# Optimization experiments

Hardware: AMD Instinct MI355X
Metric: run time of the kernel (lower is better)

The kernel has to match this reference:

```python
import jax, jax.numpy as jnp
import numpy as np

B, N, D = 32, 1024, 512
NUM_CLASSES = 4
LN_EPS = 1e-5


def _layer_norm(x, g, b):
    mu = jnp.mean(x, axis=-1, keepdims=True)
    var = jnp.mean(jnp.square(x - mu), axis=-1, keepdims=True)
    return (x - mu) * jax.lax.rsqrt(var + LN_EPS) * g + b


def setup_inputs() -> dict:
    key = jax.random.key(0)
    ks = jax.random.split(key, 8)
    s = 0.05
    inp = {
        "sc_matrix": jax.random.uniform(ks[0], (B, N, N), dtype=jnp.float32),
        # GCN encoder params
        "W1": jax.random.normal(ks[1], (N, D), dtype=jnp.float32) * s,
        "b1": jnp.zeros((D,), jnp.float32),
        "W2": jax.random.normal(ks[2], (D, D), dtype=jnp.float32) * s,
        "b2": jnp.zeros((D,), jnp.float32),
        "ln_g": jnp.ones((D,), jnp.float32),
        "ln_b": jnp.zeros((D,), jnp.float32),
        # classifier params
        "Wc1": jax.random.normal(ks[3], (D, 128), dtype=jnp.float32) * s,
        "bc1": jnp.zeros((128,), jnp.float32),
        "g1": jnp.ones((128,), jnp.float32),
        "t1": jnp.zeros((128,), jnp.float32),
        "Wc2": jax.random.normal(ks[4], (128, 64), dtype=jnp.float32) * s,
        "bc2": jnp.zeros((64,), jnp.float32),
        "g2": jnp.ones((64,), jnp.float32),
        "t2": jnp.zeros((64,), jnp.float32),
        "Wc3": jax.random.normal(ks[5], (64, NUM_CLASSES), dtype=jnp.float32) * s,
        "bc3": jnp.zeros((NUM_CLASSES,), jnp.float32),
    }
    return inp


def reference(sc_matrix, W1, b1, W2, b2, ln_g, ln_b,
              Wc1, bc1, g1, t1, Wc2, bc2, g2, t2, Wc3, bc3):
    # Every entry of sc_matrix is nonzero, so the edge list covers all (i,j)
    # pairs incl. self-loops; GCN message passing == dense normalized matmul.
    # PyG gcn_norm: deg[j] = sum_i A[i,j]; out = D^-1/2 A^T D^-1/2 h.
    A = sc_matrix                              # [B,N,N], A[b,i,j] = edge i->j
    deg = jnp.sum(A, axis=-2)                  # col sums, [B,N]
    dis = jnp.where(deg > 0, jax.lax.rsqrt(deg), 0.0)   # deg^{-1/2}
    An = jnp.swapaxes(A, -1, -2) * dis[:, :, None] * dis[:, None, :]  # [B,N,N]

    x = sc_matrix                              # node features = SC rows [B,N,N]
    h = jax.nn.relu(jnp.matmul(An, jnp.matmul(x, W1)) + b1)   # conv1+relu [B,N,D]
    h = jnp.matmul(An, jnp.matmul(h, W2)) + b2                # conv2      [B,N,D]
    z = _layer_norm(h, ln_g, ln_b)

    z_pooled = jnp.mean(z, axis=1)             # [B,D]

    c = jax.nn.relu(_layer_norm(z_pooled @ Wc1 + bc1, g1, t1))
    c = jax.nn.relu(_layer_norm(c @ Wc2 + bc2, g2, t2))
    logits = c @ Wc3 + bc3                     # [B,num_classes]
    return (logits, z_pooled)
```

## Files before the change

### kernel.cpp

```cpp
#include <hip/hip_runtime.h>
#include <hip/hip_bf16.h>

#define B_ 32
#define N_ 1024
#define D_ 512
#define LN_EPS 1e-5f

using bf16 = __bf16;
using bf16x4 = __attribute__((ext_vector_type(4))) __bf16;
using bf16x8 = __attribute__((ext_vector_type(8))) __bf16;
using floatx4 = __attribute__((ext_vector_type(4))) float;

__device__ __forceinline__ void gld16(const bf16* gp, bf16* lp) {
  __builtin_amdgcn_global_load_lds(
      (const __attribute__((address_space(1))) void*)gp,
      (__attribute__((address_space(3))) void*)lp, 16, 0, 0);
}

__global__ __launch_bounds__(256) void k_pre(const float* __restrict__ A,
                                             float* __restrict__ deg_part,
                                             bf16* __restrict__ Abf,
                                             const float* __restrict__ W1,
                                             bf16* __restrict__ W1t,
                                             const float* __restrict__ W2,
                                             bf16* __restrict__ W2t) {
  int blk = blockIdx.x;
  int t = threadIdx.x;
  if (blk < 512) {
    int b = blk >> 4;
    int rc = blk & 15;
    int r0 = rc * 64;
    const float* p = A + (size_t)b * N_ * N_ + (size_t)r0 * N_ + t * 4;
    bf16* op = Abf + (size_t)b * N_ * N_ + (size_t)r0 * N_ + t * 4;
    float4 acc = {0.f, 0.f, 0.f, 0.f};
    #pragma unroll 4
    for (int i = 0; i < 64; ++i) {
      float4 v = *(const float4*)(p + (size_t)i * N_);
      acc.x += v.x; acc.y += v.y; acc.z += v.z; acc.w += v.w;
      bf16x4 o = {(bf16)v.x, (bf16)v.y, (bf16)v.z, (bf16)v.w};
      *(bf16x4*)(op + (size_t)i * N_) = o;
    }
    *(float4*)(deg_part + ((size_t)rc * B_ + b) * N_ + t * 4) = acc;
  } else {
    __shared__ float tile[64][65];
    blk -= 512;
    const float* in; bf16* outp; int R, C, c0, r0;
    if (blk < 128) {
      in = W1; outp = W1t; R = N_; C = D_;
      c0 = (blk & 7) * 64; r0 = (blk >> 3) * 64;
    } else {
      blk -= 128;
      in = W2; outp = W2t; R = D_; C = D_;
      c0 = (blk & 7) * 64; r0 = (blk >> 3) * 64;
    }
    #pragma unroll
    for (int cc = 0; cc < 4; ++cc) {
      int idx = cc * 256 + t;
      int r = idx >> 4, c4 = (idx & 15) << 2;
      const float4 v = *(const float4*)(in + (size_t)(r0 + r) * C + c0 + c4);
      tile[r][c4 + 0] = v.x; tile[r][c4 + 1] = v.y;
      tile[r][c4 + 2] = v.z; tile[r][c4 + 3] = v.w;
    }
    __syncthreads();
    #pragma unroll
    for (int cc = 0; cc < 4; ++cc) {
      int idx = cc * 256 + t;
      int c = idx >> 4, r4 = (idx & 15) << 2;
      bf16* dst = outp + (size_t)(c0 + c) * R + r0 + r4;
      #pragma unroll
      for (int e = 0; e < 4; ++e) dst[e] = (bf16)tile[r4 + e][c];
    }
  }
}

__global__ __launch_bounds__(256) void k_build(const bf16* __restrict__ Abf,
                                               const float* __restrict__ deg_part,
                                               bf16* __restrict__ Anbf) {
  __shared__ float tile[64][65];
  __shared__ float disI[64], disJ[64];
  int b = blockIdx.z;
  int i0 = blockIdx.x * 64;
  int j0 = blockIdx.y * 64;
  int t = threadIdx.x;
  const bf16* Ab = Abf + (size_t)b * N_ * N_;
  bf16* Anb = Anbf + (size_t)b * N_ * N_;
  if (t < 64) {
    float v = 0.f;
    #pragma unroll
    for (int rc = 0; rc < 16; ++rc)
      v += deg_part[((size_t)rc * B_ + b) * N_ + i0 + t];
    disI[t] = v > 0.f ? rsqrtf(v) : 0.f;
  } else if (t < 128) {
    float v = 0.f;
    #pragma unroll
    for (int rc = 0; rc < 16; ++rc)
      v += deg_part[((size_t)rc * B_ + b) * N_ + j0 + (t - 64)];
    disJ[t - 64] = v > 0.f ? rsqrtf(v) : 0.f;
  }
  #pragma unroll
  for (int cc = 0; cc < 2; ++cc) {
    int idx = cc * 256 + t;
    int r = idx >> 3;
    int c8 = (idx & 7) << 3;
    bf16x8 v = *(const bf16x8*)(Ab + (size_t)(j0 + r) * N_ + i0 + c8);
    #pragma unroll
    for (int e = 0; e < 8; ++e) tile[r][c8 + e] = (float)v[e];
  }
  __syncthreads();
  #pragma unroll
  for (int cc = 0; cc < 2; ++cc) {
    int idx = cc * 256 + t;
    int ii = idx >> 3;
    int jj8 = (idx & 7) << 3;
    float di = disI[ii];
    bf16x8 o;
    #pragma unroll
    for (int e = 0; e < 8; ++e)
      o[e] = (bf16)(tile[jj8 + e][ii] * di * disJ[jj8 + e]);
    *(bf16x8*)(Anb + (size_t)(i0 + ii) * N_ + j0 + jj8) = o;
  }
}

template <bool BIAS, bool RELU>
__global__ __launch_bounds__(512, 2) void k_gemm8(
    const bf16* __restrict__ Abase, size_t strideA,
    const bf16* __restrict__ Btbase, size_t strideBt,
    bf16* __restrict__ Cbase, size_t strideC,
    const float* __restrict__ bias, int Nn, int K) {
  __shared__ __align__(16) bf16 smem[65536];
  bf16* sAp = smem;
  bf16* sBp = smem + 32768;

  int nxy = gridDim.x * gridDim.y;
  int L = blockIdx.z * nxy + blockIdx.y * gridDim.x + blockIdx.x;
  int b = (L & 7) + 8 * (L / (nxy * 8));
  int inner = (L >> 3) % nxy;
  int n0 = (inner % gridDim.x) * 256;
  int m0 = (inner / gridDim.x) * 256;
  const bf16* A = Abase + (size_t)b * strideA;
  const bf16* Bt = Btbase + (size_t)b * strideBt;
  int t = threadIdx.x;
  int lane = t & 63;
  int wid = t >> 6;
  int wm = wid >> 2, wn = wid & 3;
  int l16 = lane & 15, q = lane >> 4;
  int xorb = l16 & 7;
  int ck0 = ((q ^ xorb) << 3);
  int ck1 = (((q + 4) ^ xorb) << 3);
  int r0 = t >> 3;
  int csrc = (((t & 7) ^ (r0 & 7)) << 3);
  const bf16* ag = A + (size_t)(m0 + r0) * K + csrc;
  const bf16* bg = Bt + (size_t)(n0 + ((r0 >> 5) << 6) + (r0 & 31)) * K + csrc;
  bf16* al = sAp + (size_t)t * 8;
  bf16* bl = sBp + (size_t)t * 8;

#define STAGE_A(bf_, hf_, kt_)                                                 \
  { gld16(ag + (size_t)((hf_) * 64) * K + (kt_),                               \
          al + (bf_) * 16384 + (hf_) * 8192);                                  \
    gld16(ag + (size_t)(128 + (hf_) * 64) * K + (kt_),                         \
          al + (bf_) * 16384 + (hf_) * 8192 + 4096); }
#define STAGE_B(bf_, hf_, kt_)                                                 \
  { gld16(bg + (size_t)((hf_) * 32) * K + (kt_),                               \
          bl + (bf_) * 16384 + (hf_) * 8192);                                  \
    gld16(bg + (size_t)(128 + (hf_) * 32) * K + (kt_),                         \
          bl + (bf_) * 16384 + (hf_) * 8192 + 4096); }

  floatx4 acc[8][4];
  #pragma unroll
  for (int i = 0; i < 8; ++i)
    #pragma unroll
    for (int j = 0; j < 4; ++j) acc[i][j] = (floatx4){0.f, 0.f, 0.f, 0.f};

  bf16x8 a[4][2];
  bf16x8 bq[4][2];
  const bf16* arow = sAp + (wm * 64 + l16) * 64;
  const bf16* brow = sBp + (wn * 32 + l16) * 64;

#define RD_A(bf_, mq_)                                                         \
  _Pragma("unroll") for (int i = 0; i < 4; ++i) {                              \
    a[i][0] = *(const bf16x8*)(arow + (bf_) * 16384 + (mq_) * 8192 +           \
                               i * 1024 + ck0);                                \
    a[i][1] = *(const bf16x8*)(arow + (bf_) * 16384 + (mq_) * 8192 +           \
                               i * 1024 + ck1);                                \
  }
#define RD_B(bf_, nq_)                                                         \
  _Pragma("unroll") for (int j = 0; j < 2; ++j) {                              \
    bq[(nq_) * 2 + j][0] = *(const bf16x8*)(brow + (bf_) * 16384 +             \
                                            (nq_) * 8192 + j * 1024 + ck0);    \
    bq[(nq_) * 2 + j][1] = *(const bf16x8*)(brow + (bf_) * 16384 +             \
                                            (nq_) * 8192 + j * 1024 + ck1);    \
  }
#define MFMA_Q(mq_, nq_)                                                       \
  _Pragma("unroll") for (int i = 0; i < 4; ++i)                                \
    _Pragma("unroll") for (int j = 0; j < 2; ++j) {                            \
      acc[(mq_) * 4 + i][(nq_) * 2 + j] =                                      \
          __builtin_amdgcn_mfma_f32_16x16x32_bf16(                             \
              a[i][0], bq[(nq_) * 2 + j][0],                                   \
              acc[(mq_) * 4 + i][(nq_) * 2 + j], 0, 0, 0);                     \
      acc[(mq_) * 4 + i][(nq_) * 2 + j] =                                      \
          __builtin_amdgcn_mfma_f32_16x16x32_bf16(                             \
              a[i][1], bq[(nq_) * 2 + j][1],                                   \
              acc[(mq_) * 4 + i][(nq_) * 2 + j], 0, 0, 0);                     \
    }
#define BARRIER __builtin_amdgcn_s_barrier()
#define LGKM0                                                                  \
  do {                                                                         \
    asm volatile("s_waitcnt lgkmcnt(0)" ::: "memory");                         \
    __builtin_amdgcn_sched_barrier(0);                                         \
  } while (0)
#define VMCNT(n_) asm volatile("s_waitcnt vmcnt(" #n_ ")" ::: "memory")

  STAGE_A(0, 0, 0); STAGE_B(0, 0, 0); STAGE_A(0, 1, 0); STAGE_B(0, 1, 0);
  STAGE_A(1, 0, 64); STAGE_B(1, 0, 64);
  VMCNT(4);
  BARRIER;
  int NI = K >> 7;
  for (int it = 0; it < NI; ++it) {
    int kb = it << 7;
    int k1 = kb + 64;
    int k2 = kb + 128; bool p2 = k2 < K;
    int k3 = kb + 192; bool p3 = k3 < K;
    bool lastit = (it == NI - 1);
    RD_A(0, 0); RD_B(0, 0);
    STAGE_A(1, 1, k1);
    BARRIER; LGKM0;
    __builtin_amdgcn_s_setprio(1); MFMA_Q(0, 0); __builtin_amdgcn_s_setprio(0);
    BARRIER;
    RD_B(0, 1);
    STAGE_B(1, 1, k1);
    BARRIER; LGKM0;
    __builtin_amdgcn_s_setprio(1); MFMA_Q(0, 1); __builtin_amdgcn_s_setprio(0);
    BARRIER;
    RD_A(0, 1);
    if (p2) STAGE_A(0, 0, k2);
    BARRIER; LGKM0;
    __builtin_amdgcn_s_setprio(1); MFMA_Q(1, 0); __builtin_amdgcn_s_setprio(0);
    BARRIER;
    if (p2) STAGE_B(0, 0, k2);
    if (lastit) { VMCNT(0); } else { VMCNT(4); }
    BARRIER; LGKM0;
    __builtin_amdgcn_s_setprio(1); MFMA_Q(1, 1); __builtin_amdgcn_s_setprio(0);
    BARRIER;
    RD_A(1, 0); RD_B(1, 0);
    if (p2) STAGE_A(0, 1, k2);
    BARRIER; LGKM0;
    __builtin_amdgcn_s_setprio(1); MFMA_Q(0, 0); __builtin_amdgcn_s_setprio(0);
    BARRIER;
    RD_B(1, 1);
    if (p2) STAGE_B(0, 1, k2);
    BARRIER; LGKM0;
    __builtin_amdgcn_s_setprio(1); MFMA_Q(0, 1); __builtin_amdgcn_s_setprio(0);
    BARRIER;
    RD_A(1, 1);
    if (p3) STAGE_A(1, 0, k3);
    BARRIER; LGKM0;
    __builtin_amdgcn_s_setprio(1); MFMA_Q(1, 0); __builtin_amdgcn_s_setprio(0);
    BARRIER;
    if (p3) STAGE_B(1, 0, k3);
    if (lastit) { VMCNT(0); } else { VMCNT(4); }
    BARRIER; LGKM0;
    __builtin_amdgcn_s_setprio(1); MFMA_Q(1, 1); __builtin_amdgcn_s_setprio(0);
    BARRIER;
  }

  bf16* C = Cbase + (size_t)b * strideC;
  #pragma unroll
  for (int h = 0; h < 2; ++h) {
    BARRIER;
    if (wm == h) {
      #pragma unroll
      for (int fm = 0; fm < 8; ++fm)
        #pragma unroll
        for (int fn = 0; fn < 4; ++fn)
          #pragma unroll
          for (int r = 0; r < 4; ++r) {
            float v = acc[fm][fn][r];
            if (BIAS) v += bias[n0 + wn * 64 + fn * 16 + l16];
            if (RELU) v = v > 0.f ? v : 0.f;
            smem[(fm * 16 + q * 4 + r) * 264 + wn * 64 + fn * 16 + l16] =
                (bf16)v;
          }
    }
    BARRIER;
    #pragma unroll
    for (int i = 0; i < 8; ++i) {
      int idx = i * 512 + t;
      int row = idx >> 5;
      int c8 = (idx & 31) << 3;
      bf16x8 vv = *(const bf16x8*)(smem + row * 264 + c8);
      *(bf16x8*)(C + (size_t)(m0 + h * 128 + row) * Nn + n0 + c8) = vv;
    }
  }
#undef STAGE_A
#undef STAGE_B
#undef RD_A
#undef RD_B
#undef MFMA_Q
#undef BARRIER
#undef LGKM0
#undef VMCNT
}

__global__ __launch_bounds__(256) void k_lnpool(const bf16* __restrict__ H2,
                                                const float* __restrict__ g,
                                                const float* __restrict__ be,
                                                float* __restrict__ zp_part) {
  int b = blockIdx.y;
  int rx = blockIdx.x;
  int r0 = rx * 64;
  int t = threadIdx.x, lane = t & 63, w = t >> 6;
  float ge[8], bee[8];
  #pragma unroll
  for (int e = 0; e < 8; ++e) { ge[e] = g[lane * 8 + e]; bee[e] = be[lane * 8 + e]; }
  float acc[8] = {0, 0, 0, 0, 0, 0, 0, 0};
  for (int rr = 0; rr < 16; ++rr) {
    int row = r0 + w * 16 + rr;
    const bf16* p = H2 + ((size_t)b * N_ + row) * D_ + lane * 8;
    bf16x8 hv = *(const bf16x8*)p;
    float x[8];
    float s = 0.f;
    #pragma unroll
    for (int e = 0; e < 8; ++e) { x[e] = (float)hv[e]; s += x[e]; }
    #pragma unroll
    for (int off = 32; off; off >>= 1) s += __shfl_xor(s, off);
    float mu = s * (1.f / 512.f);
    float ss = 0.f;
    #pragma unroll
    for (int e = 0; e < 8; ++e) { float d = x[e] - mu; ss += d * d; }
    #pragma unroll
    for (int off = 32; off; off >>= 1) ss += __shfl_xor(ss, off);
    float rs = rsqrtf(ss * (1.f / 512.f) + LN_EPS);
    #pragma unroll
    for (int e = 0; e < 8; ++e) acc[e] += (x[e] - mu) * rs * ge[e] + bee[e];
  }
  __shared__ float part[4][512];
  #pragma unroll
  for (int e = 0; e < 8; ++e) part[w][lane * 8 + e] = acc[e];
  __syncthreads();
  #pragma unroll
  for (int k = 0; k < 2; ++k) {
    int d = t + k * 256;
    float s4 = part[0][d] + part[1][d] + part[2][d] + part[3][d];
    zp_part[((size_t)rx * B_ + b) * D_ + d] = s4;
  }
}

__global__ __launch_bounds__(128) void k_cls(
    const float* __restrict__ zp_part,
    const float* __restrict__ Wc1, const float* __restrict__ bc1,
    const float* __restrict__ g1, const float* __restrict__ t1,
    const float* __restrict__ Wc2, const float* __restrict__ bc2,
    const float* __restrict__ g2, const float* __restrict__ t2,
    const float* __restrict__ Wc3, const float* __restrict__ bc3,
    float* __restrict__ out) {
  __shared__ float z[512];
  __shared__ float c1s[128];
  __shared__ float c2s[64];
  __shared__ float red[128];
  int b = blockIdx.x, t = threadIdx.x;
  #pragma unroll
  for (int k = 0; k < 4; ++k) {
    int d = t + k * 128;
    float s = 0.f;
    #pragma unroll
    for (int rx = 0; rx < 16; ++rx)
      s += zp_part[((size_t)rx * B_ + b) * D_ + d];
    float v = s * (1.f / 1024.f);
    z[d] = v;
    out[128 + b * 512 + d] = v;
  }
  __syncthreads();
  float y = bc1[t];
  for (int d = 0; d < 512; ++d) y += z[d] * Wc1[d * 128 + t];
  red[t] = y;
  __syncthreads();
  float mu = 0.f;
  for (int k = 0; k < 128; ++k) mu += red[k];
  mu *= (1.f / 128.f);
  float var = 0.f;
  for (int k = 0; k < 128; ++k) { float dd = red[k] - mu; var += dd * dd; }
  var *= (1.f / 128.f);
  float c = (y - mu) * rsqrtf(var + LN_EPS) * g1[t] + t1[t];
  c1s[t] = c > 0.f ? c : 0.f;
  __syncthreads();
  if (t < 64) {
    float y2 = bc2[t];
    for (int k = 0; k < 128; ++k) y2 += c1s[k] * Wc2[k * 64 + t];
    red[t] = y2;
  }
  __syncthreads();
  if (t < 64) {
    float mu2 = 0.f;
    for (int k = 0; k < 64; ++k) mu2 += red[k];
    mu2 *= (1.f / 64.f);
    float v2 = 0.f;
    for (int k = 0; k < 64; ++k) { float dd = red[k] - mu2; v2 += dd * dd; }
    v2 *= (1.f / 64.f);
    float cc = (red[t] - mu2) * rsqrtf(v2 + LN_EPS) * g2[t] + t2[t];
    c2s[t] = cc > 0.f ? cc : 0.f;
  }
  __syncthreads();
  if (t < 4) {
    float y3 = bc3[t];
    for (int k = 0; k < 64; ++k) y3 += c2s[k] * Wc3[k * 4 + t];
    out[b * 4 + t] = y3;
  }
}

extern "C" void kernel_launch(void* const* d_in, const int* in_sizes, int n_in,
                              void* d_out, int out_size, void* d_ws, size_t ws_size,
                              hipStream_t stream) {
  const float* A   = (const float*)d_in[0];
  const float* W1  = (const float*)d_in[1];
  const float* b1  = (const float*)d_in[2];
  const float* W2  = (const float*)d_in[3];
  const float* b2  = (const float*)d_in[4];
  const float* lng = (const float*)d_in[5];
  const float* lnb = (const float*)d_in[6];
  const float* Wc1 = (const float*)d_in[7];
  const float* bc1 = (const float*)d_in[8];
  const float* g1  = (const float*)d_in[9];
  const float* t1  = (const float*)d_in[10];
  const float* Wc2 = (const float*)d_in[11];
  const float* bc2 = (const float*)d_in[12];
  const float* g2  = (const float*)d_in[13];
  const float* t2  = (const float*)d_in[14];
  const float* Wc3 = (const float*)d_in[15];
  const float* bc3 = (const float*)d_in[16];
  float* out = (float*)d_out;

  char* ws = (char*)d_ws;
  size_t off = 0;
  auto alloc = [&](size_t bytes) {
    char* p = ws + off;
    off += (bytes + 255) & ~(size_t)255;
    return p;
  };
  float* deg_part = (float*)alloc((size_t)16 * B_ * N_ * 4);
  float* zp_part  = (float*)alloc((size_t)16 * B_ * D_ * 4);
  bf16* Anbf  = (bf16*)alloc((size_t)B_ * N_ * N_ * 2);
  bf16* W1t   = (bf16*)alloc((size_t)D_ * N_ * 2);
  bf16* W2t   = (bf16*)alloc((size_t)D_ * D_ * 2);
  bf16* T12t  = (bf16*)alloc((size_t)B_ * D_ * N_ * 2);
  bf16* H1    = (bf16*)alloc((size_t)B_ * N_ * D_ * 2);
  bf16* Abf   = (bf16*)alloc((size_t)B_ * N_ * N_ * 2);
  bf16* H2    = Abf;


  k_pre<<<704, 256, 0, stream>>>(A, deg_part, Abf, W1, W1t, W2, W2t);
  k_build<<<dim3(16, 16, B_), 256, 0, stream>>>(Abf, deg_part, Anbf);

  k_gemm8<false, false><<<dim3(4, 2, B_), 512, 0, stream>>>(
      W1t, 0, Abf, (size_t)N_ * N_, T12t, (size_t)D_ * N_, nullptr, N_, N_);
  k_gemm8<true, true><<<dim3(2, 4, B_), 512, 0, stream>>>(
      Anbf, (size_t)N_ * N_, T12t, (size_t)D_ * N_, H1, (size_t)N_ * D_, b1, D_, N_);
  k_gemm8<false, false><<<dim3(4, 2, B_), 512, 0, stream>>>(
      W2t, 0, H1, (size_t)N_ * D_, T12t, (size_t)D_ * N_, nullptr, N_, D_);
  k_gemm8<true, false><<<dim3(2, 4, B_), 512, 0, stream>>>(
      Anbf, (size_t)N_ * N_, T12t, (size_t)D_ * N_, H2, (size_t)N_ * D_, b2, D_, N_);

  k_lnpool<<<dim3(16, B_), 256, 0, stream>>>(H2, lng, lnb, zp_part);
  k_cls<<<B_, 128, 0, stream>>>(zp_part, Wc1, bc1, g1, t1, Wc2, bc2, g2, t2,
                                Wc3, bc3, out);
}
```

Before: 431.6 us.

## Replace pipelined 256x256 GEMM with simple single-buffered 128x256 tile kernel

Replaces the 512-thread, double-buffered, barrier-interleaved GEMM with a 256-thread kernel using 128x256 tiles and one LDS buffer per K-step. It loads a K-slice, synchronises, runs the MFMAs, then synchronises again. Grids double in size, and LDS use drops so more blocks can be resident. In exchange it gives up the overlap of global loads with MFMA work and the priority scheduling.

```diff
diff --git a/kernel.cpp b/kernel.cpp
--- a/kernel.cpp
+++ b/kernel.cpp
@@ -122,183 +122,99 @@
 }
 
 template <bool BIAS, bool RELU>
-__global__ __launch_bounds__(512, 2) void k_gemm8(
+__global__ __launch_bounds__(256, 2) void k_gemm(
     const bf16* __restrict__ Abase, size_t strideA,
     const bf16* __restrict__ Btbase, size_t strideBt,
     bf16* __restrict__ Cbase, size_t strideC,
     const float* __restrict__ bias, int Nn, int K) {
-  __shared__ __align__(16) bf16 smem[65536];
-  bf16* sAp = smem;
-  bf16* sBp = smem + 32768;
-
+  __shared__ __align__(16) bf16 smem[24576];
+  bf16* sA = smem;
+  bf16* sB = smem + 8192;
   int nxy = gridDim.x * gridDim.y;
   int L = blockIdx.z * nxy + blockIdx.y * gridDim.x + blockIdx.x;
   int b = (L & 7) + 8 * (L / (nxy * 8));
   int inner = (L >> 3) % nxy;
   int n0 = (inner % gridDim.x) * 256;
-  int m0 = (inner / gridDim.x) * 256;
+  int m0 = (inner / gridDim.x) * 128;
+
   const bf16* A = Abase + (size_t)b * strideA;
   const bf16* Bt = Btbase + (size_t)b * strideBt;
   int t = threadIdx.x;
-  int lane = t & 63;
-  int wid = t >> 6;
-  int wm = wid >> 2, wn = wid & 3;
+  int lane = t & 63, wid = t >> 6;
+  int wm = (wid >> 1) * 64, wn = (wid & 1) * 128;
   int l16 = lane & 15, q = lane >> 4;
+
+  int rowoff = lane >> 3;
+  int schunk = (lane & 7) ^ rowoff;
+  const bf16* agp = A + (size_t)(m0 + wid * 32 + rowoff) * K + schunk * 8;
+  const bf16* bgp = Bt + (size_t)(n0 + wid * 64 + rowoff) * K + schunk * 8;
+  bf16* alp = &sA[wid * 2048 + lane * 8];
+  bf16* blp = &sB[wid * 4096 + lane * 8];
+
   int xorb = l16 & 7;
-  int ck0 = ((q ^ xorb) << 3);
-  int ck1 = (((q + 4) ^ xorb) << 3);
-  int r0 = t >> 3;
-  int csrc = (((t & 7) ^ (r0 & 7)) << 3);
-  const bf16* ag = A + (size_t)(m0 + r0) * K + csrc;
-  const bf16* bg = Bt + (size_t)(n0 + ((r0 >> 5) << 6) + (r0 & 31)) * K + csrc;
-  bf16* al = sAp + (size_t)t * 8;
-  bf16* bl = sBp + (size_t)t * 8;
-
-#define STAGE_A(bf_, hf_, kt_)                                                 \
-  { gld16(ag + (size_t)((hf_) * 64) * K + (kt_),                               \
-          al + (bf_) * 16384 + (hf_) * 8192);                                  \
-    gld16(ag + (size_t)(128 + (hf_) * 64) * K + (kt_),                         \
-          al + (bf_) * 16384 + (hf_) * 8192 + 4096); }
-#define STAGE_B(bf_, hf_, kt_)                                                 \
-  { gld16(bg + (size_t)((hf_) * 32) * K + (kt_),                               \
-          bl + (bf_) * 16384 + (hf_) * 8192);                                  \
-    gld16(bg + (size_t)(128 + (hf_) * 32) * K + (kt_),                         \
-          bl + (bf_) * 16384 + (hf_) * 8192 + 4096); }
-
-  floatx4 acc[8][4];
-  #pragma unroll
-  for (int i = 0; i < 8; ++i)
-    #pragma unroll
-    for (int j = 0; j < 4; ++j) acc[i][j] = (floatx4){0.f, 0.f, 0.f, 0.f};
-
-  bf16x8 a[4][2];
-  bf16x8 bq[4][2];
-  const bf16* arow = sAp + (wm * 64 + l16) * 64;
-  const bf16* brow = sBp + (wn * 32 + l16) * 64;
-
-#define RD_A(bf_, mq_)                                                         \
-  _Pragma("unroll") for (int i = 0; i < 4; ++i) {                              \
-    a[i][0] = *(const bf16x8*)(arow + (bf_) * 16384 + (mq_) * 8192 +           \
-                               i * 1024 + ck0);                                \
-    a[i][1] = *(const bf16x8*)(arow + (bf_) * 16384 + (mq_) * 8192 +           \
-                               i * 1024 + ck1);                                \
-  }
-#define RD_B(bf_, nq_)                                                         \
-  _Pragma("unroll") for (int j = 0; j < 2; ++j) {                              \
-    bq[(nq_) * 2 + j][0] = *(const bf16x8*)(brow + (bf_) * 16384 +             \
-                                            (nq_) * 8192 + j * 1024 + ck0);    \
-    bq[(nq_) * 2 + j][1] = *(const bf16x8*)(brow + (bf_) * 16384 +             \
-                                            (nq_) * 8192 + j * 1024 + ck1);    \
-  }
-#define MFMA_Q(mq_, nq_)                                                       \
-  _Pragma("unroll") for (int i = 0; i < 4; ++i)                                \
-    _Pragma("unroll") for (int j = 0; j < 2; ++j) {                            \
-      acc[(mq_) * 4 + i][(nq_) * 2 + j] =                                      \
-          __builtin_amdgcn_mfma_f32_16x16x32_bf16(                             \
-              a[i][0], bq[(nq_) * 2 + j][0],                                   \
-              acc[(mq_) * 4 + i][(nq_) * 2 + j], 0, 0, 0);                     \
-      acc[(mq_) * 4 + i][(nq_) * 2 + j] =                                      \
-          __builtin_amdgcn_mfma_f32_16x16x32_bf16(                             \
-              a[i][1], bq[(nq_) * 2 + j][1],                                   \
-              acc[(mq_) * 4 + i][(nq_) * 2 + j], 0, 0, 0);                     \
-    }
-#define BARRIER __builtin_amdgcn_s_barrier()
-#define LGKM0                                                                  \
-  do {                                                                         \
-    asm volatile("s_waitcnt lgkmcnt(0)" ::: "memory");                         \
-    __builtin_amdgcn_sched_barrier(0);                                         \
-  } while (0)
-#define VMCNT(n_) asm volatile("s_waitcnt vmcnt(" #n_ ")" ::: "memory")
-
-  STAGE_A(0, 0, 0); STAGE_B(0, 0, 0); STAGE_A(0, 1, 0); STAGE_B(0, 1, 0);
-  STAGE_A(1, 0, 64); STAGE_B(1, 0, 64);
-  VMCNT(4);
-  BARRIER;
-  int NI = K >> 7;
-  for (int it = 0; it < NI; ++it) {
-    int kb = it << 7;
-    int k1 = kb + 64;
-    int k2 = kb + 128; bool p2 = k2 < K;
-    int k3 = kb + 192; bool p3 = k3 < K;
-    bool lastit = (it == NI - 1);
-    RD_A(0, 0); RD_B(0, 0);
-    STAGE_A(1, 1, k1);
-    BARRIER; LGKM0;
-    __builtin_amdgcn_s_setprio(1); MFMA_Q(0, 0); __builtin_amdgcn_s_setprio(0);
-    BARRIER;
-    RD_B(0, 1);
-    STAGE_B(1, 1, k1);
-    BARRIER; LGKM0;
-    __builtin_amdgcn_s_setprio(1); MFMA_Q(0, 1); __builtin_amdgcn_s_setprio(0);
-    BARRIER;
-    RD_A(0, 1);
-    if (p2) STAGE_A(0, 0, k2);
-    BARRIER; LGKM0;
-    __builtin_amdgcn_s_setprio(1); MFMA_Q(1, 0); __builtin_amdgcn_s_setprio(0);
-    BARRIER;
-    if (p2) STAGE_B(0, 0, k2);
-    if (lastit) { VMCNT(0); } else { VMCNT(4); }
-    BARRIER; LGKM0;
-    __builtin_amdgcn_s_setprio(1); MFMA_Q(1, 1); __builtin_amdgcn_s_setprio(0);
-    BARRIER;
-    RD_A(1, 0); RD_B(1, 0);
-    if (p2) STAGE_A(0, 1, k2);
-    BARRIER; LGKM0;
-    __builtin_amdgcn_s_setprio(1); MFMA_Q(0, 0); __builtin_amdgcn_s_setprio(0);
-    BARRIER;
-    RD_B(1, 1);
-    if (p2) STAGE_B(0, 1, k2);
-    BARRIER; LGKM0;
-    __builtin_amdgcn_s_setprio(1); MFMA_Q(0, 1); __builtin_amdgcn_s_setprio(0);
-    BARRIER;
-    RD_A(1, 1);
-    if (p3) STAGE_A(1, 0, k3);
-    BARRIER; LGKM0;
-    __builtin_amdgcn_s_setprio(1); MFMA_Q(1, 0); __builtin_amdgcn_s_setprio(0);
-    BARRIER;
-    if (p3) STAGE_B(1, 0, k3);
-    if (lastit) { VMCNT(0); } else { VMCNT(4); }
-    BARRIER; LGKM0;
-    __builtin_amdgcn_s_setprio(1); MFMA_Q(1, 1); __builtin_amdgcn_s_setprio(0);
-    BARRIER;
+
+  floatx4 acc[4][8];
+  #pragma unroll
+  for (int i = 0; i < 4; ++i)
+    #pragma unroll
+    for (int j = 0; j < 8; ++j) acc[i][j] = (floatx4){0.f, 0.f, 0.f, 0.f};
+
+  for (int kt = 0; kt < K; kt += 64) {
+    #pragma unroll
+    for (int s = 0; s < 4; ++s)
+      gld16(agp + (size_t)s * 8 * K + kt, alp + s * 512);
+    #pragma unroll
+    for (int s = 0; s < 8; ++s)
+      gld16(bgp + (size_t)s * 8 * K + kt, blp + s * 512);
+    __syncthreads();
+    #pragma unroll
+    for (int h = 0; h < 2; ++h) {
+      int cko = ((q + 4 * h) ^ xorb) * 8;
+      bf16x8 af[4], bfr[8];
+      #pragma unroll
+      for (int mt = 0; mt < 4; ++mt)
+        af[mt] = *(const bf16x8*)(&sA[(wm + mt * 16 + l16) * 64 + cko]);
+      #pragma unroll
+      for (int nt = 0; nt < 8; ++nt)
+        bfr[nt] = *(const bf16x8*)(&sB[(wn + nt * 16 + l16) * 64 + cko]);
+      #pragma unroll
+      for (int mt = 0; mt < 4; ++mt)
+        #pragma unroll
+        for (int nt = 0; nt < 8; ++nt)
+          acc[mt][nt] = __builtin_amdgcn_mfma_f32_16x16x32_bf16(
+              af[mt], bfr[nt], acc[mt][nt], 0, 0, 0);
+    }
+    __syncthreads();
   }
 
   bf16* C = Cbase + (size_t)b * strideC;
   #pragma unroll
   for (int h = 0; h < 2; ++h) {
-    BARRIER;
-    if (wm == h) {
-      #pragma unroll
-      for (int fm = 0; fm < 8; ++fm)
+    if ((wid >> 1) == h) {
+      #pragma unroll
+      for (int mt = 0; mt < 4; ++mt)
         #pragma unroll
-        for (int fn = 0; fn < 4; ++fn)
+        for (int nt = 0; nt < 8; ++nt)
           #pragma unroll
           for (int r = 0; r < 4; ++r) {
-            float v = acc[fm][fn][r];
-            if (BIAS) v += bias[n0 + wn * 64 + fn * 16 + l16];
+            float v = acc[mt][nt][r];
+            int col = wn + nt * 16 + l16;
+            if (BIAS) v += bias[n0 + col];
             if (RELU) v = v > 0.f ? v : 0.f;
-            smem[(fm * 16 + q * 4 + r) * 264 + wn * 64 + fn * 16 + l16] =
-                (bf16)v;
+            smem[(mt * 16 + q * 4 + r) * 264 + col] = (bf16)v;
           }
     }
-    BARRIER;
+    __syncthreads();
     #pragma unroll
     for (int i = 0; i < 8; ++i) {
-      int idx = i * 512 + t;
+      int idx = i * 256 + t;
       int row = idx >> 5;
       int c8 = (idx & 31) << 3;
       bf16x8 vv = *(const bf16x8*)(smem + row * 264 + c8);
-      *(bf16x8*)(C + (size_t)(m0 + h * 128 + row) * Nn + n0 + c8) = vv;
-    }
-  }
-#undef STAGE_A
-#undef STAGE_B
-#undef RD_A
-#undef RD_B
-#undef MFMA_Q
-#undef BARRIER
-#undef LGKM0
-#undef VMCNT
+      *(bf16x8*)(C + (size_t)(m0 + h * 64 + row) * Nn + n0 + c8) = vv;
+    }
+    if (h == 0) __syncthreads();
+  }
 }
 
 __global__ __launch_bounds__(256) void k_lnpool(const bf16* __restrict__ H2,
@@ -450,13 +366,13 @@
   k_pre<<<704, 256, 0, stream>>>(A, deg_part, Abf, W1, W1t, W2, W2t);
   k_build<<<dim3(16, 16, B_), 256, 0, stream>>>(Abf, deg_part, Anbf);
 
-  k_gemm8<false, false><<<dim3(4, 2, B_), 512, 0, stream>>>(
+  k_gemm<false, false><<<dim3(4, 4, B_), 256, 0, stream>>>(
       W1t, 0, Abf, (size_t)N_ * N_, T12t, (size_t)D_ * N_, nullptr, N_, N_);
-  k_gemm8<true, true><<<dim3(2, 4, B_), 512, 0, stream>>>(
+  k_gemm<true, true><<<dim3(2, 8, B_), 256, 0, stream>>>(
       Anbf, (size_t)N_ * N_, T12t, (size_t)D_ * N_, H1, (size_t)N_ * D_, b1, D_, N_);
-  k_gemm8<false, false><<<dim3(4, 2, B_), 512, 0, stream>>>(
+  k_gemm<false, false><<<dim3(4, 4, B_), 256, 0, stream>>>(
       W2t, 0, H1, (size_t)N_ * D_, T12t, (size_t)D_ * N_, nullptr, N_, D_);
-  k_gemm8<true, false><<<dim3(2, 4, B_), 512, 0, stream>>>(
+  k_gemm<true, false><<<dim3(2, 8, B_), 256, 0, stream>>>(
       Anbf, (size_t)N_ * N_, T12t, (size_t)D_ * N_, H2, (size_t)N_ * D_, b2, D_, N_);
 
   k_lnpool<<<dim3(16, B_), 256, 0, stream>>>(H2, lng, lnb, zp_part);
```

Result: faster. 418.4 us (-3.1%).
